# Kernel optimization log

Measured on AMD Instinct MI355X. Metric: run time of the kernel, lower is better.

## Reference

```python
import jax, jax.numpy as jnp
import numpy as np

KS = 2        # kernel_size
DIL = 1       # dilation
FILTERS = 512
Z_DIM = 128
B, C, T = 8, 512, 4096
TZ = T + 2 * (KS - 1)


def _conv1d(x, w, b):
    # x: (B, L, Cin), w: (ks, Cin, Cout) -> VALID conv, channels-last (keras Conv1D)
    y = jax.lax.conv_general_dilated(x, w, window_strides=(1,), padding='VALID',
                                     dimension_numbers=('NWC', 'WIO', 'NWC'))
    return y + b


def _adaptor(z, w1, b1, w2, b2):
    return _conv1d(jax.nn.relu(_conv1d(z, w1, b1)), w2, b2)


def setup_inputs() -> dict:
    key = jax.random.key(0)
    ks = jax.random.split(key, 10)
    lim = np.sqrt(6.0 / FILTERS)
    u = lambda k, shp: jax.random.uniform(k, shp, jnp.float32, -lim, lim)
    return {
        'x': jax.random.normal(ks[0], (B, C, T), jnp.float32),
        'z': jax.random.normal(ks[1], (B, TZ, Z_DIM), jnp.float32),
        'ww1': u(ks[2], (KS, Z_DIM, FILTERS)), 'wb1': jnp.zeros((FILTERS,), jnp.float32),
        'ww2': u(ks[3], (KS, FILTERS, FILTERS)), 'wb2': jnp.zeros((FILTERS,), jnp.float32),
        'bw1': u(ks[4], (KS, Z_DIM, FILTERS)), 'bb1': jnp.zeros((FILTERS,), jnp.float32),
        'bw2': u(ks[5], (KS, FILTERS, FILTERS)), 'bb2': jnp.zeros((FILTERS,), jnp.float32),
    }


def reference(x, z, ww1, wb1, ww2, wb2, bw1, bb1, bw2, bb2):
    m = x.shape[1]
    t = x.shape[2]
    pad = DIL * (KS - 1)
    xp = jnp.pad(x, ((0, 0), (0, 0), (0, pad)))
    end = t + pad
    # im2col-style unfold: (B, C*KS, T)
    xu = jnp.concatenate([xp[:, :, pad - i * DIL: end - i * DIL] for i in range(KS)], axis=1)
    weights = _adaptor(z, ww1, wb1, ww2, wb2)   # (B, T, F)
    bias = _adaptor(z, bw1, bb1, bw2, bb2)      # (B, T, F)
    y = jnp.matmul(xu, weights)                 # (B, C*KS, F)
    return y[:, :m, :] + bias[:, :m, :]
```

## Files before the change

kernel.cpp:

```cpp
#include <hip/hip_runtime.h>

typedef short short8 __attribute__((ext_vector_type(8)));
typedef float float4v __attribute__((ext_vector_type(4)));
typedef __attribute__((address_space(1))) const unsigned int gu32;
typedef __attribute__((address_space(3))) unsigned int lu32;

__device__ __forceinline__ unsigned short f2bf(float f) {
  unsigned int u = __builtin_bit_cast(unsigned int, f);
  u += 0x7FFFu + ((u >> 16) & 1u);
  return (unsigned short)(u >> 16);
}
__device__ __forceinline__ float bf2f(unsigned short s) {
  return __builtin_bit_cast(float, (unsigned int)s << 16);
}

__global__ __launch_bounds__(256) void prep_w(
    const float* __restrict__ ww1, const float* __restrict__ ww2,
    const float* __restrict__ bw1, const float* __restrict__ bw2,
    const float* __restrict__ z,
    unsigned short* __restrict__ w1T, unsigned short* __restrict__ w2T,
    unsigned short* __restrict__ b1T, unsigned short* __restrict__ b2T,
    unsigned short* __restrict__ zb)
{
  int i = blockIdx.x * 256 + threadIdx.x;
  if (i < 131072) {
    int n = i & 511, k = i >> 9;
    w1T[n * 256 + k] = f2bf(ww1[i]);
  } else if (i < 655360) {
    int j = i - 131072; int n = j & 511, k = j >> 9;
    w2T[n * 1024 + k] = f2bf(ww2[j]);
  } else if (i < 786432) {
    int j = i - 655360; int n = j & 511, k = j >> 9;
    b1T[n * 256 + k] = f2bf(bw1[j]);
  } else if (i < 1310720) {
    int j = i - 786432; int n = j & 511, k = j >> 9;
    b2T[n * 1024 + k] = f2bf(bw2[j]);
  } else {
    int j = i - 1310720;
    zb[j] = f2bf(z[j]);
  }
}

template<int BM, int BN, bool RELU, bool OBF16, bool TRANS, bool SPLITK, int NH, bool ROWPACK>
__device__ __forceinline__ void gemm_core(
    int bx, int by, int bz, int nzTot, unsigned short* smem,
    const unsigned short* __restrict__ A,
    const unsigned short* __restrict__ A2,
    const unsigned short* __restrict__ Bt,
    const float* __restrict__ biasv,
    void* __restrict__ outp,
    void* __restrict__ outp2,
    int M, int Kchunk, int RPB, int EXTRA, int BSCALE,
    int nHalf, int bRowMask,
    long long bStrideB, long long outBatchStride, int outLd)
{
  constexpr int WM = BM / 2, WN = BN / 2;
  constexpr int NI = WM / 16, NJ = WN / 16;
  constexpr int AI = BM / 64;
  constexpr int BI = BN / 64;
  constexpr int SA1 = BM * 32, SB1 = BN * 32;
  unsigned short* sB0 = smem + NH * SA1;

  const int tid  = threadIdx.x;
  const int lane = tid & 63;
  const int wave = tid >> 6;
  const int wm = wave >> 1, wn = wave & 1;
  const int lr = lane & 15, quad = lane >> 4;

  const int r0 = bx * BM;
  const int n0 = by * BN;
  const int bb = r0 / RPB;
  const int Ktot = SPLITK ? Kchunk * nzTot : Kchunk;
  const int kOff = SPLITK ? bz * Kchunk : 0;
  const long long bOffB = (long long)bb * bStrideB;
  const unsigned short* Ae = (nHalf && n0 >= nHalf) ? A2 : A;

  const int srow = lane >> 2;
  const int sg = (lane & 3) ^ (srow & 3);
  const unsigned short* gA[AI]; unsigned short* ldsA[AI];
#pragma unroll
  for (int c = 0; c < AI; ++c) {
    int instr = c * 4 + wave;
    int row = instr * 16 + srow;
    int r = r0 + row; if (r > M - 1) r = M - 1;
    gA[c] = Ae + ((long long)r + (long long)(r / RPB) * EXTRA) * BSCALE + kOff + sg * 8;
    ldsA[c] = smem + instr * 512;
  }
  const unsigned short* gB[BI]; unsigned short* ldsB[BI];
#pragma unroll
  for (int c = 0; c < BI; ++c) {
    int instr = c * 4 + wave;
    int row = instr * 16 + srow;
    gB[c] = Bt + (long long)((n0 + row) & bRowMask) * Ktot + bOffB + kOff + sg * 8;
    ldsB[c] = sB0 + instr * 512;
  }

  int aoff[NI], boff[NJ];
#pragma unroll
  for (int i = 0; i < NI; ++i) {
    int rr = wm * WM + i * 16 + lr;
    aoff[i] = rr * 32 + ((quad ^ (rr & 3)) * 8);
  }
#pragma unroll
  for (int j = 0; j < NJ; ++j) {
    int rr = wn * WN + j * 16 + lr;
    boff[j] = rr * 32 + ((quad ^ (rr & 3)) * 8);
  }

  float4v acc[NI][NJ];
  const float4v z4 = {0.f, 0.f, 0.f, 0.f};
#pragma unroll
  for (int i = 0; i < NI; ++i)
#pragma unroll
    for (int j = 0; j < NJ; ++j) acc[i][j] = z4;

  for (int k0 = 0; k0 < Kchunk; k0 += 32 * NH) {
#pragma unroll
    for (int h = 0; h < NH; ++h) {
#pragma unroll
      for (int c = 0; c < AI; ++c)
        __builtin_amdgcn_global_load_lds((gu32*)(gA[c] + k0 + h * 32),
                                         (lu32*)(ldsA[c] + h * SA1), 16, 0, 0);
#pragma unroll
      for (int c = 0; c < BI; ++c)
        __builtin_amdgcn_global_load_lds((gu32*)(gB[c] + k0 + h * 32),
                                         (lu32*)(ldsB[c] + h * SB1), 16, 0, 0);
    }
    __syncthreads();
#pragma unroll
    for (int h = 0; h < NH; ++h) {
      short8 af[NI], bfr[NJ];
#pragma unroll
      for (int i = 0; i < NI; ++i) af[i] = *(const short8*)(smem + h * SA1 + aoff[i]);
#pragma unroll
      for (int j = 0; j < NJ; ++j) bfr[j] = *(const short8*)(sB0 + h * SB1 + boff[j]);
#pragma unroll
      for (int i = 0; i < NI; ++i)
#pragma unroll
        for (int j = 0; j < NJ; ++j)
          acc[i][j] = __builtin_amdgcn_mfma_f32_16x16x32_bf16(af[i], bfr[j], acc[i][j], 0, 0, 0);
    }
    __syncthreads();
  }

  if (TRANS) {
    unsigned short* Ts = smem;
    const int t0l = r0 - bb * RPB;
#pragma unroll
    for (int p = 0; p < 2; ++p) {
      if (wn == p) {
#pragma unroll
        for (int j = 0; j < NJ; ++j) {
          int frl = j * 16 + lr;
          float bv = biasv[n0 + p * WN + frl];
#pragma unroll
          for (int i = 0; i < NI; ++i) {
            int tr = wm * WM + i * 16 + quad * 4;
            unsigned long long pk = 0;
#pragma unroll
            for (int g = 0; g < 4; ++g) {
              float vv = acc[i][j][g] + bv;
              if (RELU) vv = fmaxf(vv, 0.f);
              pk |= (unsigned long long)f2bf(vv) << (16 * g);
            }
            *(unsigned long long*)(Ts + frl * (BM + 8) + tr) = pk;
          }
        }
      }
      __syncthreads();
      int frl = tid >> 2, sgg = tid & 3;
      unsigned short* dst = (unsigned short*)outp + (long long)bb * outBatchStride
                          + (long long)(n0 + p * WN + frl) * outLd + t0l + sgg * (BM / 4);
      const unsigned short* srcp = Ts + frl * (BM + 8) + sgg * (BM / 4);
#pragma unroll
      for (int u = 0; u < BM / 32; ++u)
        *(uint4*)(dst + u * 8) = *(const uint4*)(srcp + u * 8);
      __syncthreads();
    }
  } else if (ROWPACK) {
    constexpr int BNP = BN + 8;
    constexpr int TPR = 256 / BM;
    constexpr int EPT = BN / TPR;
    void* op = (SPLITK && bz) ? outp2 : outp;
    unsigned short* R = smem;
#pragma unroll
    for (int j = 0; j < NJ; ++j) {
      int cc = wn * WN + j * 16 + lr;
#pragma unroll
      for (int i = 0; i < NI; ++i) {
        int rrb = wm * WM + i * 16 + quad * 4;
#pragma unroll
        for (int g = 0; g < 4; ++g)
          R[(rrb + g) * BNP + cc] = f2bf(acc[i][j][g]);
      }
    }
    __syncthreads();
    int rloc = tid / TPR, part = tid % TPR;
    unsigned short* dstp = (unsigned short*)op + (long long)(r0 + rloc) * outLd + n0 + part * EPT;
    const unsigned short* srcp = R + rloc * BNP + part * EPT;
#pragma unroll
    for (int u = 0; u < EPT / 8; ++u)
      *(uint4*)(dstp + u * 8) = *(const uint4*)(srcp + u * 8);
  } else {
    void* op = (SPLITK && bz) ? outp2 : outp;
#pragma unroll
    for (int j = 0; j < NJ; ++j) {
      int n_g = n0 + wn * WN + j * 16 + lr;
      float bv = biasv ? biasv[n_g] : 0.f;
#pragma unroll
      for (int i = 0; i < NI; ++i) {
        int r_base = r0 + wm * WM + i * 16 + quad * 4;
#pragma unroll
        for (int g = 0; g < 4; ++g) {
          int r_g = r_base + g;
          if (r_g >= M) continue;
          float v = acc[i][j][g] + bv;
          if (RELU) v = fmaxf(v, 0.f);
          long long oidx = (long long)r_g * outLd + n_g;
          if (OBF16) ((unsigned short*)op)[oidx] = f2bf(v);
          else       ((float*)op)[oidx] = v;
        }
      }
    }
  }
}

template<int BM, int BN, bool RELU, bool OBF16, bool TRANS, bool SPLITK, int NH, bool ROWPACK>
__global__ __launch_bounds__(256)
void gemm_bt(const unsigned short* __restrict__ A,
             const unsigned short* __restrict__ A2,
             const unsigned short* __restrict__ Bt,
             const float* __restrict__ biasv,
             void* __restrict__ outp,
             void* __restrict__ outp2,
             int M, int Kchunk, int RPB, int EXTRA, int BSCALE,
             int nHalf, int bRowMask,
             long long bStrideB, long long outBatchStride, int outLd)
{
  constexpr int STAGE = NH * (BM * 32 + BN * 32);
  constexpr int REPK = TRANS ? (BN / 2) * (BM + 8) : (ROWPACK ? BM * (BN + 8) : 0);
  constexpr int SMEMN = (REPK > STAGE) ? REPK : STAGE;
  __shared__ unsigned short smem[SMEMN];
  gemm_core<BM, BN, RELU, OBF16, TRANS, SPLITK, NH, ROWPACK>(
      blockIdx.x, blockIdx.y, blockIdx.z, gridDim.z, smem,
      A, A2, Bt, biasv, outp, outp2,
      M, Kchunk, RPB, EXTRA, BSCALE, nHalf, bRowMask,
      bStrideB, outBatchStride, outLd);
}

__global__ __launch_bounds__(256) void mega(
    const float* __restrict__ x,
    const unsigned short* __restrict__ zb,
    const unsigned short* __restrict__ w1T,
    const unsigned short* __restrict__ b1T,
    const float* __restrict__ wb1,
    const float* __restrict__ bb1,
    unsigned short* __restrict__ h1T,
    unsigned short* __restrict__ h1b,
    unsigned short* __restrict__ xs,
    unsigned short* __restrict__ xz,
    float* __restrict__ rs)
{
  __shared__ unsigned short smem[8704];
  int b = blockIdx.x;
  if (b < 1024) {
    gemm_core<128, 128, true, true, true, false, 1, false>(
        b & 255, b >> 8, 0, 1, smem,
        zb, nullptr, w1T, wb1, h1T, nullptr,
        32768, 256, 4096, 2, 128, 0, 0xFFFF, 0, 512ll * 4096, 4096);
  } else if (b < 1284) {
    int idx = b - 1024;
    gemm_core<64, 128, true, true, false, false, 1, false>(
        idx % 65, idx / 65, 0, 1, smem,
        zb, nullptr, b1T, bb1, h1b, nullptr,
        4104, 256, 513, 3585, 128, 0, 0xFFFF, 0, 0, 512);
  } else {
    float* red = (float*)smem;
    long long r = b - 1284;
    const float* xr = x + r * 4096;
    int t0 = threadIdx.x * 16;
    float v[17];
    const float4* xr4 = (const float4*)(xr + t0);
#pragma unroll
    for (int q = 0; q < 4; ++q) {
      float4 f = xr4[q];
      v[q * 4] = f.x; v[q * 4 + 1] = f.y; v[q * 4 + 2] = f.z; v[q * 4 + 3] = f.w;
    }
    v[16] = (t0 + 16 < 4096) ? xr[t0 + 16] : 0.f;
    unsigned int spk[8], zpk[8];
    float sum = 0.f;
#pragma unroll
    for (int q = 0; q < 8; ++q) {
      unsigned short s0 = f2bf(v[2 * q + 1]);
      unsigned short s1 = f2bf(v[2 * q + 2]);
      sum += bf2f(s0);
      sum += bf2f(s1);
      spk[q] = (unsigned int)s0 | ((unsigned int)s1 << 16);
      unsigned short z0 = (t0 == 0 && q == 0) ? (unsigned short)0 : f2bf(v[2 * q]);
      unsigned short z1 = f2bf(v[2 * q + 1]);
      zpk[q] = (unsigned int)z0 | ((unsigned int)z1 << 16);
    }
    *(uint4*)(xs + r * 4096 + t0)     = *(uint4*)(spk);
    *(uint4*)(xs + r * 4096 + t0 + 8) = *(uint4*)(spk + 4);
    *(uint4*)(xz + r * 4096 + t0)     = *(uint4*)(zpk);
    *(uint4*)(xz + r * 4096 + t0 + 8) = *(uint4*)(zpk + 4);
#pragma unroll
    for (int off = 32; off > 0; off >>= 1) sum += __shfl_down(sum, off);
    if ((threadIdx.x & 63) == 0) red[threadIdx.x >> 6] = sum;
    __syncthreads();
    if (threadIdx.x == 0) rs[r] = red[0] + red[1] + red[2] + red[3];
  }
}

__global__ __launch_bounds__(256) void final_gemm3(
    const unsigned short* __restrict__ p0,
    const unsigned short* __restrict__ p1,
    const unsigned short* __restrict__ h1b,
    const unsigned short* __restrict__ w2T,
    const unsigned short* __restrict__ b2T,
    const float* __restrict__ rs,
    const float* __restrict__ wb2,
    const float* __restrict__ bb2,
    float* __restrict__ out)
{
  constexpr int SA1 = 64 * 32, SB1 = 64 * 32;
  __shared__ unsigned short smem[4 * SA1 + 4 * SB1];
  const int tid = threadIdx.x;
  const int lane = tid & 63, wave = tid >> 6;
  const int wm = wave >> 1, wn = wave & 1;
  const int lr = lane & 15, quad = lane >> 4;
  const int r0 = blockIdx.x * 64, n0 = blockIdx.y * 64;

  const int srow = lane >> 2;
  const int sg = (lane & 3) ^ (srow & 3);
  const int row = wave * 16 + srow;
  const int rA = r0 + row;
  const int rB = n0 + row;
  const unsigned short* aP[3] = {
    p0 + (long long)rA * 1024 + sg * 8,
    p1 + (long long)rA * 1024 + sg * 8,
    h1b + ((long long)rA + (rA >> 9)) * 512 + sg * 8 };
  const unsigned short* bP[3] = {
    w2T + (long long)rB * 1024 + sg * 8,
    w2T + (long long)rB * 1024 + sg * 8,
    b2T + (long long)rB * 1024 + sg * 8 };
  unsigned short* ldsA = smem + wave * 512;
  unsigned short* ldsB = smem + 4 * SA1 + wave * 512;

  int aoff[2], boff[2];
#pragma unroll
  for (int i = 0; i < 2; ++i) {
    int rr = wm * 32 + i * 16 + lr;
    aoff[i] = rr * 32 + ((quad ^ (rr & 3)) * 8);
    int nn = wn * 32 + i * 16 + lr;
    boff[i] = 4 * SA1 + nn * 32 + ((quad ^ (nn & 3)) * 8);
  }

  float4v acc[2][2];
  const float4v z4 = {0.f, 0.f, 0.f, 0.f};
  acc[0][0] = z4; acc[0][1] = z4; acc[1][0] = z4; acc[1][1] = z4;

  for (int k0 = 0; k0 < 3072; k0 += 128) {
    int seg = k0 >> 10;
    int kk = k0 & 1023;
#pragma unroll
    for (int h = 0; h < 4; ++h) {
      __builtin_amdgcn_global_load_lds((gu32*)(aP[seg] + kk + h * 32),
                                       (lu32*)(ldsA + h * SA1), 16, 0, 0);
      __builtin_amdgcn_global_load_lds((gu32*)(bP[seg] + kk + h * 32),
                                       (lu32*)(ldsB + h * SB1), 16, 0, 0);
    }
    __syncthreads();
#pragma unroll
    for (int h = 0; h < 4; ++h) {
      short8 af[2], bfr[2];
      af[0] = *(const short8*)(smem + h * SA1 + aoff[0]);
      af[1] = *(const short8*)(smem + h * SA1 + aoff[1]);
      bfr[0] = *(const short8*)(smem + h * SB1 + boff[0]);
      bfr[1] = *(const short8*)(smem + h * SB1 + boff[1]);
#pragma unroll
      for (int i = 0; i < 2; ++i)
#pragma unroll
        for (int j = 0; j < 2; ++j)
          acc[i][j] = __builtin_amdgcn_mfma_f32_16x16x32_bf16(af[i], bfr[j], acc[i][j], 0, 0, 0);
    }
    __syncthreads();
  }

#pragma unroll
  for (int j = 0; j < 2; ++j) {
    int n_g = n0 + wn * 32 + j * 16 + lr;
    float w2b = wb2[n_g], bbv = bb2[n_g];
#pragma unroll
    for (int i = 0; i < 2; ++i) {
      int rb = r0 + wm * 32 + i * 16 + quad * 4;
#pragma unroll
      for (int g = 0; g < 4; ++g) {
        int r_g = rb + g;
        out[(long long)r_g * 512 + n_g] = acc[i][j][g] + rs[r_g] * w2b + bbv;
      }
    }
  }
}

extern "C" void kernel_launch(void* const* d_in, const int* in_sizes, int n_in,
                              void* d_out, int out_size, void* d_ws, size_t ws_size,
                              hipStream_t stream) {
  const float* x   = (const float*)d_in[0];
  const float* z   = (const float*)d_in[1];
  const float* ww1 = (const float*)d_in[2];
  const float* wb1 = (const float*)d_in[3];
  const float* ww2 = (const float*)d_in[4];
  const float* wb2 = (const float*)d_in[5];
  const float* bw1 = (const float*)d_in[6];
  const float* bb1 = (const float*)d_in[7];
  const float* bw2 = (const float*)d_in[8];
  const float* bb2 = (const float*)d_in[9];

  char* ws = (char*)d_ws;
  unsigned short* xs  = (unsigned short*)ws; ws += 16777216ll * 2;
  unsigned short* xz  = (unsigned short*)ws; ws += 16777216ll * 2;
  unsigned short* zb  = (unsigned short*)ws; ws += 4196352ll  * 2;
  unsigned short* h1T = (unsigned short*)ws; ws += 16777216ll * 2;
  unsigned short* h1b = (unsigned short*)ws; ws += 2101248ll  * 2;
  unsigned short* w2T = (unsigned short*)ws; ws += 524288ll * 2;
  unsigned short* b2T = (unsigned short*)ws; ws += 524288ll * 2;
  float* rs = (float*)ws;                    ws += 4096ll * 4;
  char* tail = ws;
  unsigned short* w1T = (unsigned short*)tail;
  unsigned short* b1T = (unsigned short*)tail + 131072;
  unsigned short* p0  = zb;
  unsigned short* p1  = (unsigned short*)tail;

  prep_w<<<21512, 256, 0, stream>>>(ww1, ww2, bw1, bw2, z, w1T, w2T, b1T, b2T, zb);
  mega<<<5380, 256, 0, stream>>>(x, zb, w1T, b1T, wb1, bb1, h1T, h1b, xs, xz, rs);
  gemm_bt<128, 64, false, true, false, true, 2, true><<<dim3(32, 16, 2), 256, 0, stream>>>(
      xs, xz, h1T, nullptr, p0, p1,
      4096, 2048, 512, 0, 4096, 512, 511, 512ll * 4096, 0, 1024);
  final_gemm3<<<dim3(64, 8), 256, 0, stream>>>(
      p0, p1, h1b, w2T, b2T, rs, wb2, bb2, (float*)d_out);
}
```

Before: 259.9 us.

## Double-buffer LDS staging in split-K and final GEMMs, widen split-K tile

```diff
diff --git a/kernel.cpp b/kernel.cpp
--- a/kernel.cpp
+++ b/kernel.cpp
@@ -41,7 +41,8 @@
   }
 }
 
-template<int BM, int BN, bool RELU, bool OBF16, bool TRANS, bool SPLITK, int NH, bool ROWPACK>
+template<int BM, int BN, bool RELU, bool OBF16, bool TRANS, bool SPLITK, int NH,
+         bool ROWPACK, bool DBUF>
 __device__ __forceinline__ void gemm_core(
     int bx, int by, int bz, int nzTot, unsigned short* smem,
     const unsigned short* __restrict__ A,
@@ -114,33 +115,64 @@
 #pragma unroll
     for (int j = 0; j < NJ; ++j) acc[i][j] = z4;
 
-  for (int k0 = 0; k0 < Kchunk; k0 += 32 * NH) {
-#pragma unroll
-    for (int h = 0; h < NH; ++h) {
+  if (DBUF) {
+    auto stage_ch = [&](int kk, int h) {
 #pragma unroll
       for (int c = 0; c < AI; ++c)
-        __builtin_amdgcn_global_load_lds((gu32*)(gA[c] + k0 + h * 32),
+        __builtin_amdgcn_global_load_lds((gu32*)(gA[c] + kk),
                                          (lu32*)(ldsA[c] + h * SA1), 16, 0, 0);
 #pragma unroll
       for (int c = 0; c < BI; ++c)
-        __builtin_amdgcn_global_load_lds((gu32*)(gB[c] + k0 + h * 32),
+        __builtin_amdgcn_global_load_lds((gu32*)(gB[c] + kk),
                                          (lu32*)(ldsB[c] + h * SB1), 16, 0, 0);
-    }
+    };
+    stage_ch(0, 0);
     __syncthreads();
-#pragma unroll
-    for (int h = 0; h < NH; ++h) {
+    int rbuf = 0;
+    for (int k0 = 0; k0 < Kchunk; k0 += 32) {
+      if (k0 + 32 < Kchunk) stage_ch(k0 + 32, rbuf ^ 1);
       short8 af[NI], bfr[NJ];
 #pragma unroll
-      for (int i = 0; i < NI; ++i) af[i] = *(const short8*)(smem + h * SA1 + aoff[i]);
-#pragma unroll
-      for (int j = 0; j < NJ; ++j) bfr[j] = *(const short8*)(sB0 + h * SB1 + boff[j]);
+      for (int i = 0; i < NI; ++i) af[i] = *(const short8*)(smem + rbuf * SA1 + aoff[i]);
+#pragma unroll
+      for (int j = 0; j < NJ; ++j) bfr[j] = *(const short8*)(sB0 + rbuf * SB1 + boff[j]);
 #pragma unroll
       for (int i = 0; i < NI; ++i)
 #pragma unroll
         for (int j = 0; j < NJ; ++j)
           acc[i][j] = __builtin_amdgcn_mfma_f32_16x16x32_bf16(af[i], bfr[j], acc[i][j], 0, 0, 0);
-    }
-    __syncthreads();
+      __syncthreads();
+      rbuf ^= 1;
+    }
+  } else {
+    for (int k0 = 0; k0 < Kchunk; k0 += 32 * NH) {
+#pragma unroll
+      for (int h = 0; h < NH; ++h) {
+#pragma unroll
+        for (int c = 0; c < AI; ++c)
+          __builtin_amdgcn_global_load_lds((gu32*)(gA[c] + k0 + h * 32),
+                                           (lu32*)(ldsA[c] + h * SA1), 16, 0, 0);
+#pragma unroll
+        for (int c = 0; c < BI; ++c)
+          __builtin_amdgcn_global_load_lds((gu32*)(gB[c] + k0 + h * 32),
+                                           (lu32*)(ldsB[c] + h * SB1), 16, 0, 0);
+      }
+      __syncthreads();
+#pragma unroll
+      for (int h = 0; h < NH; ++h) {
+        short8 af[NI], bfr[NJ];
+#pragma unroll
+        for (int i = 0; i < NI; ++i) af[i] = *(const short8*)(smem + h * SA1 + aoff[i]);
+#pragma unroll
+        for (int j = 0; j < NJ; ++j) bfr[j] = *(const short8*)(sB0 + h * SB1 + boff[j]);
+#pragma unroll
+        for (int i = 0; i < NI; ++i)
+#pragma unroll
+          for (int j = 0; j < NJ; ++j)
+            acc[i][j] = __builtin_amdgcn_mfma_f32_16x16x32_bf16(af[i], bfr[j], acc[i][j], 0, 0, 0);
+      }
+      __syncthreads();
+    }
   }
 
   if (TRANS) {
@@ -178,29 +210,38 @@
       __syncthreads();
     }
   } else if (ROWPACK) {
+    constexpr int P  = (BM > 64) ? 2 : 1;
+    constexpr int RP = BM / P;
     constexpr int BNP = BN + 8;
-    constexpr int TPR = 256 / BM;
+    constexpr int TPR = 256 / RP;
     constexpr int EPT = BN / TPR;
     void* op = (SPLITK && bz) ? outp2 : outp;
     unsigned short* R = smem;
 #pragma unroll
-    for (int j = 0; j < NJ; ++j) {
-      int cc = wn * WN + j * 16 + lr;
-#pragma unroll
-      for (int i = 0; i < NI; ++i) {
-        int rrb = wm * WM + i * 16 + quad * 4;
-#pragma unroll
-        for (int g = 0; g < 4; ++g)
-          R[(rrb + g) * BNP + cc] = f2bf(acc[i][j][g]);
-      }
-    }
-    __syncthreads();
-    int rloc = tid / TPR, part = tid % TPR;
-    unsigned short* dstp = (unsigned short*)op + (long long)(r0 + rloc) * outLd + n0 + part * EPT;
-    const unsigned short* srcp = R + rloc * BNP + part * EPT;
-#pragma unroll
-    for (int u = 0; u < EPT / 8; ++u)
-      *(uint4*)(dstp + u * 8) = *(const uint4*)(srcp + u * 8);
+    for (int p = 0; p < P; ++p) {
+      if (P == 1 || wm == p) {
+#pragma unroll
+        for (int j = 0; j < NJ; ++j) {
+          int cc = wn * WN + j * 16 + lr;
+#pragma unroll
+          for (int i = 0; i < NI; ++i) {
+            int rl = (P == 1 ? wm * WM : 0) + i * 16 + quad * 4;
+#pragma unroll
+            for (int g = 0; g < 4; ++g)
+              R[(rl + g) * BNP + cc] = f2bf(acc[i][j][g]);
+          }
+        }
+      }
+      __syncthreads();
+      int rloc = tid / TPR, part = tid % TPR;
+      unsigned short* dstp = (unsigned short*)op
+                           + (long long)(r0 + p * RP + rloc) * outLd + n0 + part * EPT;
+      const unsigned short* srcp = R + rloc * BNP + part * EPT;
+#pragma unroll
+      for (int u = 0; u < EPT / 8; ++u)
+        *(uint4*)(dstp + u * 8) = *(const uint4*)(srcp + u * 8);
+      if (p + 1 < P) __syncthreads();
+    }
   } else {
     void* op = (SPLITK && bz) ? outp2 : outp;
 #pragma unroll
@@ -225,7 +266,8 @@
   }
 }
 
-template<int BM, int BN, bool RELU, bool OBF16, bool TRANS, bool SPLITK, int NH, bool ROWPACK>
+template<int BM, int BN, bool RELU, bool OBF16, bool TRANS, bool SPLITK, int NH,
+         bool ROWPACK, bool DBUF>
 __global__ __launch_bounds__(256)
 void gemm_bt(const unsigned short* __restrict__ A,
              const unsigned short* __restrict__ A2,
@@ -238,10 +280,11 @@
              long long bStrideB, long long outBatchStride, int outLd)
 {
   constexpr int STAGE = NH * (BM * 32 + BN * 32);
-  constexpr int REPK = TRANS ? (BN / 2) * (BM + 8) : (ROWPACK ? BM * (BN + 8) : 0);
+  constexpr int REPK = TRANS ? (BN / 2) * (BM + 8)
+                     : (ROWPACK ? (BM > 64 ? (BM / 2) * (BN + 8) : BM * (BN + 8)) : 0);
   constexpr int SMEMN = (REPK > STAGE) ? REPK : STAGE;
   __shared__ unsigned short smem[SMEMN];
-  gemm_core<BM, BN, RELU, OBF16, TRANS, SPLITK, NH, ROWPACK>(
+  gemm_core<BM, BN, RELU, OBF16, TRANS, SPLITK, NH, ROWPACK, DBUF>(
       blockIdx.x, blockIdx.y, blockIdx.z, gridDim.z, smem,
       A, A2, Bt, biasv, outp, outp2,
       M, Kchunk, RPB, EXTRA, BSCALE, nHalf, bRowMask,
@@ -264,13 +307,13 @@
   __shared__ unsigned short smem[8704];
   int b = blockIdx.x;
   if (b < 1024) {
-    gemm_core<128, 128, true, true, true, false, 1, false>(
+    gemm_core<128, 128, true, true, true, false, 1, false, false>(
         b & 255, b >> 8, 0, 1, smem,
         zb, nullptr, w1T, wb1, h1T, nullptr,
         32768, 256, 4096, 2, 128, 0, 0xFFFF, 0, 512ll * 4096, 4096);
   } else if (b < 1284) {
     int idx = b - 1024;
-    gemm_core<64, 128, true, true, false, false, 1, false>(
+    gemm_core<64, 128, true, true, false, false, 1, false, false>(
         idx % 65, idx / 65, 0, 1, smem,
         zb, nullptr, b1T, bb1, h1b, nullptr,
         4104, 256, 513, 3585, 128, 0, 0xFFFF, 0, 0, 512);
@@ -360,24 +403,24 @@
   const float4v z4 = {0.f, 0.f, 0.f, 0.f};
   acc[0][0] = z4; acc[0][1] = z4; acc[1][0] = z4; acc[1][1] = z4;
 
-  for (int k0 = 0; k0 < 3072; k0 += 128) {
-    int seg = k0 >> 10;
-    int kk = k0 & 1023;
-#pragma unroll
-    for (int h = 0; h < 4; ++h) {
-      __builtin_amdgcn_global_load_lds((gu32*)(aP[seg] + kk + h * 32),
-                                       (lu32*)(ldsA + h * SA1), 16, 0, 0);
-      __builtin_amdgcn_global_load_lds((gu32*)(bP[seg] + kk + h * 32),
-                                       (lu32*)(ldsB + h * SB1), 16, 0, 0);
-    }
-    __syncthreads();
-#pragma unroll
-    for (int h = 0; h < 4; ++h) {
+  auto stg = [&](int k, int s) {
+    int seg = k >> 10, kk = k & 1023;
+    __builtin_amdgcn_global_load_lds((gu32*)(aP[seg] + kk), (lu32*)(ldsA + s * SA1), 16, 0, 0);
+    __builtin_amdgcn_global_load_lds((gu32*)(bP[seg] + kk), (lu32*)(ldsB + s * SB1), 16, 0, 0);
+  };
+  stg(0, 0); stg(32, 1);
+  __syncthreads();
+  int rb = 0;
+  for (int k0 = 0; k0 < 3072; k0 += 64) {
+    if (k0 + 64 < 3072) { stg(k0 + 64, (rb ^ 1) * 2); stg(k0 + 96, (rb ^ 1) * 2 + 1); }
+#pragma unroll
+    for (int h = 0; h < 2; ++h) {
+      int s = rb * 2 + h;
       short8 af[2], bfr[2];
-      af[0] = *(const short8*)(smem + h * SA1 + aoff[0]);
-      af[1] = *(const short8*)(smem + h * SA1 + aoff[1]);
-      bfr[0] = *(const short8*)(smem + h * SB1 + boff[0]);
-      bfr[1] = *(const short8*)(smem + h * SB1 + boff[1]);
+      af[0] = *(const short8*)(smem + s * SA1 + aoff[0]);
+      af[1] = *(const short8*)(smem + s * SA1 + aoff[1]);
+      bfr[0] = *(const short8*)(smem + s * SB1 + boff[0]);
+      bfr[1] = *(const short8*)(smem + s * SB1 + boff[1]);
 #pragma unroll
       for (int i = 0; i < 2; ++i)
 #pragma unroll
@@ -385,6 +428,7 @@
           acc[i][j] = __builtin_amdgcn_mfma_f32_16x16x32_bf16(af[i], bfr[j], acc[i][j], 0, 0, 0);
     }
     __syncthreads();
+    rb ^= 1;
   }
 
 #pragma unroll
@@ -393,10 +437,10 @@
     float w2b = wb2[n_g], bbv = bb2[n_g];
 #pragma unroll
     for (int i = 0; i < 2; ++i) {
-      int rb = r0 + wm * 32 + i * 16 + quad * 4;
+      int rb2 = r0 + wm * 32 + i * 16 + quad * 4;
 #pragma unroll
       for (int g = 0; g < 4; ++g) {
-        int r_g = rb + g;
+        int r_g = rb2 + g;
         out[(long long)r_g * 512 + n_g] = acc[i][j][g] + rs[r_g] * w2b + bbv;
       }
     }
@@ -434,7 +478,7 @@
 
   prep_w<<<21512, 256, 0, stream>>>(ww1, ww2, bw1, bw2, z, w1T, w2T, b1T, b2T, zb);
   mega<<<5380, 256, 0, stream>>>(x, zb, w1T, b1T, wb1, bb1, h1T, h1b, xs, xz, rs);
-  gemm_bt<128, 64, false, true, false, true, 2, true><<<dim3(32, 16, 2), 256, 0, stream>>>(
+  gemm_bt<128, 128, false, true, false, true, 2, true, true><<<dim3(32, 8, 2), 256, 0, stream>>>(
       xs, xz, h1T, nullptr, p0, p1,
       4096, 2048, 512, 0, 4096, 512, 511, 512ll * 4096, 0, 1024);
   final_gemm3<<<dim3(64, 8), 256, 0, stream>>>(
```

Measured after the change: 252.8 us. 2.7% less time.
